# Kernel optimization log

Hardware: AMD Instinct MI355X
Metric: run time of the kernel (lower is better)

The kernel has to match this reference:

```python
import jax, jax.numpy as jnp
import numpy as np

N_NODES = 50000
N_EDGES = 300000
ANNOT = 200
HID = 256
N_STEPS = 8
N_BRANCH = 2


def setup_inputs() -> dict:
    key = jax.random.key(0)
    ks = jax.random.split(key, 12)
    s = 0.05
    return {
        "x": jax.random.normal(ks[0], (N_NODES, ANNOT), dtype=jnp.float32),
        "edge_index": jax.random.randint(ks[1], (2, N_EDGES), 0, N_NODES, dtype=jnp.int32),
        "batch": jnp.zeros((N_NODES,), dtype=jnp.int32),
        "W_reduce": jax.random.normal(ks[2], (HID, ANNOT), dtype=jnp.float32) * s,
        "b_reduce": jnp.zeros((HID,), dtype=jnp.float32),
        "W_ggc": jax.random.normal(ks[3], (N_STEPS, HID, HID), dtype=jnp.float32) * s,
        "W_ih": jax.random.normal(ks[4], (3 * HID, HID), dtype=jnp.float32) * s,
        "W_hh": jax.random.normal(ks[5], (3 * HID, HID), dtype=jnp.float32) * s,
        "b_ih": jnp.zeros((3 * HID,), dtype=jnp.float32),
        "b_hh": jnp.zeros((3 * HID,), dtype=jnp.float32),
        "W_lin": jax.random.normal(ks[6], (N_BRANCH, HID), dtype=jnp.float32) * s,
        "b_lin": jnp.zeros((N_BRANCH,), dtype=jnp.float32),
    }


def _gru_cell(m, h, W_ih, W_hh, b_ih, b_hh):
    # PyTorch GRUCell: gates ordered r, z, n
    gi = m @ W_ih.T + b_ih  # [N, 3H]
    gh = h @ W_hh.T + b_hh
    i_r, i_z, i_n = jnp.split(gi, 3, axis=1)
    h_r, h_z, h_n = jnp.split(gh, 3, axis=1)
    r = jax.nn.sigmoid(i_r + h_r)
    z = jax.nn.sigmoid(i_z + h_z)
    n = jnp.tanh(i_n + r * h_n)
    return (1.0 - z) * n + z * h


def reference(x, edge_index, batch, W_reduce, b_reduce, W_ggc, W_ih, W_hh, b_ih, b_hh, W_lin, b_lin):
    del batch  # unused by forward math
    n = x.shape[0]
    src, dst = edge_index[0], edge_index[1]

    h = x @ W_reduce.T + b_reduce  # [N, H]

    def step(h, Wi):
        m = h @ Wi                                    # per-step linear [N, H]
        agg = jax.ops.segment_sum(m[src], dst, num_segments=n)  # scatter-add to targets
        h_new = _gru_cell(agg, h, W_ih, W_hh, b_ih, b_hh)
        return h_new, None

    h, _ = jax.lax.scan(step, h, W_ggc)

    out = jax.nn.relu(h) @ W_lin.T + b_lin  # [N, 2]
    return jax.nn.log_softmax(out, axis=1)
```

## Files before the change

kernel.cpp:

```cpp
#include <hip/hip_runtime.h>

typedef _Float16 f16;
typedef unsigned short u16;
typedef unsigned int u32;
typedef _Float16 f16x4 __attribute__((ext_vector_type(4)));
typedef _Float16 f16x8 __attribute__((ext_vector_type(8)));
typedef float    floatx4 __attribute__((ext_vector_type(4)));

#define N_NODES 50000
#define N_EDGES 300000
#define ANNOT   200
#define KXP     224
#define HID     256

__device__ __forceinline__ floatx4 mfma_16x16x32_f16(f16x8 a, f16x8 b, floatx4 c) {
#if defined(__HIP_DEVICE_COMPILE__)
    return __builtin_amdgcn_mfma_f32_16x16x32_f16(a, b, c, 0, 0, 0);
#else
    return c;
#endif
}
__device__ __forceinline__ void gload_lds16(const f16* g, f16* l) {
#if defined(__HIP_DEVICE_COMPILE__)
    __builtin_amdgcn_global_load_lds((const __attribute__((address_space(1))) void*)g,
                                     (__attribute__((address_space(3))) void*)l, 16, 0, 0);
#else
    (void)g; (void)l;
#endif
}

__device__ __forceinline__ float sigm(float x) { return 1.0f / (1.0f + __expf(-x)); }
__device__ __forceinline__ float tanh_fast(float x) { return 1.0f - 2.0f / (1.0f + __expf(2.0f * x)); }

__device__ __forceinline__ float bf_bits_to_f32(u16 u) {
    union { u32 i; float f; } v; v.i = ((u32)u) << 16; return v.f;
}
__device__ __forceinline__ u16 f32_to_bf_bits(float f) {
    union { float f; u32 i; } v; v.f = f;
    u32 b = v.i;
    b += 0x7FFFu + ((b >> 16) & 1u);
    return (u16)(b >> 16);
}
__device__ __forceinline__ float load_in(const void* p, long i, int flag) {
    if (flag) return ((const float*)p)[i];
    return bf_bits_to_f32(((const u16*)p)[i]);
}

__global__ void probe_dtype(const u32* __restrict__ xw, int* __restrict__ flag) {
    __shared__ int cnt;
    if (threadIdx.x == 0) cnt = 0;
    __syncthreads();
    int c = 0;
    for (int i = threadIdx.x; i < 256; i += 64) {
        u32 lo = xw[i] & 0xFFFFu;
        u32 e = (lo >> 7) & 0xFFu;
        if (e >= 105u && e <= 140u) c++;
    }
    atomicAdd(&cnt, c);
    __syncthreads();
    if (threadIdx.x == 0) flag[0] = (cnt > 128) ? 0 : 1;
}

__global__ void cvt_f16(const void* __restrict__ in, f16* __restrict__ out, int n,
                        const int* __restrict__ flagp) {
    const int flag = *flagp;
    const int i = blockIdx.x * 256 + threadIdx.x;
    if (i < n) out[i] = (f16)load_in(in, i, flag);
}

__global__ void build_wrT(const void* __restrict__ Wre, f16* __restrict__ WrT,
                          const int* __restrict__ flagp) {
    const int flag = *flagp;
    const int i = blockIdx.x * 256 + threadIdx.x;
    if (i >= 256 * KXP) return;
    const int n = i / KXP, k = i - n * KXP;
    WrT[i] = (k < ANNOT) ? (f16)load_in(Wre, (long)n * ANNOT + k, flag) : (f16)0.0f;
}

__global__ void build_bb8(const f16* __restrict__ Wc, const void* __restrict__ Whh,
                          f16* __restrict__ Bb, const int* __restrict__ flagp) {
    const int flag = *flagp;
    const int i = blockIdx.x * 256 + threadIdx.x;
    const int s = i >> 19;
    const int rem = i & 524287;
    const int row = rem >> 9;
    const int k = rem & 511;
    const int chblk = row >> 7;
    const int r = row & 127;
    const int g = r >> 5;
    const int c = r & 31;
    const int ch = chblk * 32 + c;
    f16 v = (f16)0.0f;
    if (g == 0) {
        v = (k < 256) ? Wc[(long)ch * 2048 + s * 256 + k]
                      : (f16)load_in(Whh, (long)ch * 256 + (k - 256), flag);
    } else if (g == 1) {
        v = (k < 256) ? Wc[(long)(256 + ch) * 2048 + s * 256 + k]
                      : (f16)load_in(Whh, (long)(256 + ch) * 256 + (k - 256), flag);
    } else if (g == 2) {
        if (k < 256) v = Wc[(long)(512 + ch) * 2048 + s * 256 + k];
    } else {
        if (k >= 256) v = (f16)load_in(Whh, (long)(512 + ch) * 256 + (k - 256), flag);
    }
    Bb[i] = v;
}

__global__ void build_small(const void* b_ih, const void* b_hh, const void* b_red,
                            const void* W_lin, const void* b_lin,
                            float* __restrict__ sp, const int* __restrict__ flagp) {
    const int flag = *flagp;
    const int i = blockIdx.x * 256 + threadIdx.x;
    if (i < 512) {
        sp[i] = load_in(b_ih, i, flag) + load_in(b_hh, i, flag);
    } else if (i < 768) {
        sp[i] = load_in(b_ih, 512 + (i - 512), flag);
    } else if (i < 1024) {
        sp[i] = load_in(b_hh, 512 + (i - 768), flag);
    } else if (i < 1280) {
        sp[i] = load_in(b_red, i - 1024, flag);
    } else if (i < 1792) {
        sp[i] = load_in(W_lin, i - 1280, flag);
    } else if (i < 1794) {
        sp[i] = load_in(b_lin, i - 1792, flag);
    }
}

__global__ void build_xcvt(const void* __restrict__ x, f16* __restrict__ xc,
                           const int* __restrict__ flagp) {
    const int flag = *flagp;
    const long i = (long)blockIdx.x * 256 + threadIdx.x;
    if (i >= (long)N_NODES * KXP) return;
    const long r = i / KXP;
    const int  k = (int)(i - r * KXP);
    xc[i] = (k < ANNOT) ? (f16)load_in(x, r * ANNOT + k, flag) : (f16)0.0f;
}

__global__ void zero_i32(int* __restrict__ p, int n) {
    const int i = blockIdx.x * 256 + threadIdx.x;
    if (i < n) p[i] = 0;
}
__global__ void hist_kernel(const int* __restrict__ dst, int* __restrict__ deg, int n) {
    const int e = blockIdx.x * 256 + threadIdx.x;
    if (e < n) atomicAdd(&deg[dst[e]], 1);
}
__global__ void block_sum(const int* __restrict__ deg, int* __restrict__ partial, int n) {
    __shared__ int s[256];
    const int i = blockIdx.x * 256 + threadIdx.x;
    s[threadIdx.x] = (i < n) ? deg[i] : 0;
    __syncthreads();
    for (int off = 128; off > 0; off >>= 1) {
        if (threadIdx.x < off) s[threadIdx.x] += s[threadIdx.x + off];
        __syncthreads();
    }
    if (threadIdx.x == 0) partial[blockIdx.x] = s[0];
}
__global__ void scan_partials(int* __restrict__ partial, int nb, int* __restrict__ total_out) {
    __shared__ int s[256];
    const int t = threadIdx.x;
    s[t] = (t < nb) ? partial[t] : 0;
    __syncthreads();
    for (int off = 1; off < 256; off <<= 1) {
        int v = (t >= off) ? s[t - off] : 0;
        __syncthreads();
        s[t] += v;
        __syncthreads();
    }
    if (t < nb) partial[t] = (t == 0) ? 0 : s[t - 1];
    if (t == 0) *total_out = s[255];
}
__global__ void scan_block(const int* __restrict__ deg, const int* __restrict__ partial,
                           int* __restrict__ row_off, int* __restrict__ cursor, int n) {
    __shared__ int s[256];
    const int t = threadIdx.x;
    const int i = blockIdx.x * 256 + t;
    const int v = (i < n) ? deg[i] : 0;
    s[t] = v;
    __syncthreads();
    for (int off = 1; off < 256; off <<= 1) {
        int u = (t >= off) ? s[t - off] : 0;
        __syncthreads();
        s[t] += u;
        __syncthreads();
    }
    if (i < n) {
        const int v0 = partial[blockIdx.x] + s[t] - v;
        row_off[i] = v0;
        cursor[i]  = v0;
    }
}
__global__ void fill_kernel(const int* __restrict__ src, const int* __restrict__ dst,
                            int* __restrict__ cursor, int* __restrict__ csr, int n) {
    const int e = blockIdx.x * 256 + threadIdx.x;
    if (e < n) {
        const int p = atomicAdd(&cursor[dst[e]], 1);
        csr[p] = src[e];
    }
}

__global__ __launch_bounds__(256) void mgemm(
    const f16* __restrict__ A, int lda,
    const f16* __restrict__ Bt, int ldb,
    f16* __restrict__ C, int ldc,
    const float* __restrict__ bias,
    int M, int N, int K)
{
    __shared__ __attribute__((aligned(16))) f16 As[128 * 32];
    __shared__ __attribute__((aligned(16))) f16 Bs[128 * 32];
    const int tid  = threadIdx.x;
    const int lane = tid & 63;
    const int wave = tid >> 6;
    const int bm = blockIdx.x * 128;
    const int bn = blockIdx.y * 128;
    const int wm = (wave >> 1) * 64;
    const int wn = (wave & 1) * 64;
    const int quad = lane >> 4;
    const int l16  = lane & 15;

    floatx4 acc[4][4];
#pragma unroll
    for (int i = 0; i < 4; ++i)
#pragma unroll
        for (int j = 0; j < 4; ++j) acc[i][j] = (floatx4)(0.0f);

    for (int k0 = 0; k0 < K; k0 += 32) {
        __syncthreads();
#pragma unroll
        for (int it = 0; it < 2; ++it) {
            const int ci  = it * 256 + tid;
            const int row = ci >> 2;
            const int cg  = ci & 3;
            int ga = bm + row; if (ga > M - 1) ga = M - 1;
            gload_lds16(A + (long)ga * lda + k0 + cg * 8, As + ci * 8);
            gload_lds16(Bt + (long)(bn + row) * ldb + k0 + cg * 8, Bs + ci * 8);
        }
        __syncthreads();

        f16x8 af[4], bfv[4];
#pragma unroll
        for (int i = 0; i < 4; ++i) {
            af[i]  = *(const f16x8*)(As + (wm + i * 16 + l16) * 32 + quad * 8);
            bfv[i] = *(const f16x8*)(Bs + (wn + i * 16 + l16) * 32 + quad * 8);
        }
#pragma unroll
        for (int i = 0; i < 4; ++i)
#pragma unroll
            for (int j = 0; j < 4; ++j)
                acc[i][j] = mfma_16x16x32_f16(af[i], bfv[j], acc[i][j]);
    }

#pragma unroll
    for (int i = 0; i < 4; ++i) {
        const int r0 = bm + wm + i * 16 + quad * 4;
#pragma unroll
        for (int j = 0; j < 4; ++j) {
            const int col = bn + wn + j * 16 + l16;
            const float bv = bias ? bias[col] : 0.0f;
#pragma unroll
            for (int v = 0; v < 4; ++v) {
                const int r = r0 + v;
                if (r < M) C[(long)r * ldc + col] = (f16)(acc[i][j][v] + bv);
            }
        }
    }
}

__global__ __launch_bounds__(256) void gemm_gates(
    const f16* __restrict__ agh, const f16* __restrict__ Bb,
    f16* __restrict__ agh_nxt,
    const float* __restrict__ brz, const float* __restrict__ bin,
    const float* __restrict__ bhn, int M)
{
    __shared__ __attribute__((aligned(16))) f16 As[128 * 32];
    __shared__ __attribute__((aligned(16))) f16 Bs[128 * 32];
    const int tid  = threadIdx.x;
    const int lane = tid & 63;
    const int wave = tid >> 6;
    const int bm = blockIdx.y * 128;
    const int by = blockIdx.x;
    const int wm  = (wave >> 1) * 64;
    const int chh = (wave & 1) * 16;
    const int quad = lane >> 4;
    const int l16  = lane & 15;

    floatx4 acc[4][4];
#pragma unroll
    for (int i = 0; i < 4; ++i)
#pragma unroll
        for (int j = 0; j < 4; ++j) acc[i][j] = (floatx4)(0.0f);

    for (int k0 = 0; k0 < 512; k0 += 32) {
        __syncthreads();
#pragma unroll
        for (int it = 0; it < 2; ++it) {
            const int ci  = it * 256 + tid;
            const int row = ci >> 2;
            const int cg  = ci & 3;
            int ga = bm + row; if (ga > M - 1) ga = M - 1;
            gload_lds16(agh + (long)ga * 512 + k0 + cg * 8, As + ci * 8);
            gload_lds16(Bb + (long)(by * 128 + row) * 512 + k0 + cg * 8, Bs + ci * 8);
        }
        __syncthreads();

        f16x8 af[4], bfv[4];
#pragma unroll
        for (int i = 0; i < 4; ++i) {
            af[i]  = *(const f16x8*)(As + (wm + i * 16 + l16) * 32 + quad * 8);
            bfv[i] = *(const f16x8*)(Bs + (i * 32 + chh + l16) * 32 + quad * 8);
        }
#pragma unroll
        for (int i = 0; i < 4; ++i)
#pragma unroll
            for (int j = 0; j < 4; ++j)
                acc[i][j] = mfma_16x16x32_f16(af[i], bfv[j], acc[i][j]);
    }

    const int ch = by * 32 + chh + l16;
    const float b_r  = brz[ch];
    const float b_z  = brz[256 + ch];
    const float b_in = bin[ch];
    const float b_hn = bhn[ch];
#pragma unroll
    for (int i = 0; i < 4; ++i) {
        const int r0 = bm + wm + i * 16 + quad * 4;
#pragma unroll
        for (int v = 0; v < 4; ++v) {
            const int r = r0 + v;
            if (r < M) {
                const float rg = sigm(acc[i][0][v] + b_r);
                const float zg = sigm(acc[i][1][v] + b_z);
                const float nn = tanh_fast(acc[i][2][v] + b_in + rg * (acc[i][3][v] + b_hn));
                const float ho = (float)agh[(long)r * 512 + 256 + ch];
                agh_nxt[(long)r * 512 + 256 + ch] = (f16)((1.0f - zg) * nn + zg * ho);
            }
        }
    }
}

__global__ __launch_bounds__(256) void aggregate(
    f16* __restrict__ agh, const int* __restrict__ row_off, const int* __restrict__ csr)
{
    const int node = blockIdx.x * 4 + (threadIdx.x >> 6);
    const int lane = threadIdx.x & 63;
    if (node >= N_NODES) return;
    const int e0 = row_off[node], e1 = row_off[node + 1];
    float a0 = 0.0f, a1 = 0.0f, a2 = 0.0f, a3 = 0.0f;
    for (int e = e0; e < e1; ++e) {
        const int s = csr[e];
        const f16x4 v = *(const f16x4*)(agh + (long)s * 512 + 256 + lane * 4);
        a0 += (float)v[0]; a1 += (float)v[1]; a2 += (float)v[2]; a3 += (float)v[3];
    }
    f16x4 o;
    o[0] = (f16)a0; o[1] = (f16)a1; o[2] = (f16)a2; o[3] = (f16)a3;
    *(f16x4*)(agh + (long)node * 512 + lane * 4) = o;
}

__global__ __launch_bounds__(256) void final_kernel(
    const f16* __restrict__ h, const float* __restrict__ wlin,
    const float* __restrict__ blin, void* __restrict__ out,
    const int* __restrict__ flagp)
{
    const int flag = *flagp;
    const int node = blockIdx.x * 4 + (threadIdx.x >> 6);
    const int lane = threadIdx.x & 63;
    if (node >= N_NODES) return;
    const f16* hp = h + (long)node * 512;
    float a0 = 0.0f, a1 = 0.0f;
#pragma unroll
    for (int u = 0; u < 4; ++u) {
        const int c = lane * 4 + u;
        float hv = (float)hp[c];
        hv = hv > 0.0f ? hv : 0.0f;
        a0 += hv * wlin[c];
        a1 += hv * wlin[256 + c];
    }
#pragma unroll
    for (int off = 32; off > 0; off >>= 1) {
        a0 += __shfl_down(a0, off);
        a1 += __shfl_down(a1, off);
    }
    if (lane == 0) {
        a0 += blin[0];
        a1 += blin[1];
        const float mx  = fmaxf(a0, a1);
        const float lse = mx + logf(expf(a0 - mx) + expf(a1 - mx));
        const float o0 = a0 - lse, o1 = a1 - lse;
        if (flag) {
            ((float*)out)[(long)node * 2]     = o0;
            ((float*)out)[(long)node * 2 + 1] = o1;
        } else {
            ((u16*)out)[(long)node * 2]     = f32_to_bf_bits(o0);
            ((u16*)out)[(long)node * 2 + 1] = f32_to_bf_bits(o1);
        }
    }
}

extern "C" void kernel_launch(void* const* d_in, const int* in_sizes, int n_in,
                              void* d_out, int out_size, void* d_ws, size_t ws_size,
                              hipStream_t stream)
{
    (void)in_sizes; (void)n_in; (void)out_size; (void)ws_size;
    const void* x        = d_in[0];
    const int*  ei       = (const int*)d_in[1];
    const void* W_reduce = d_in[3];
    const void* b_reduce = d_in[4];
    const void* W_ggc    = d_in[5];
    const void* W_ih     = d_in[6];
    const void* W_hh     = d_in[7];
    const void* b_ih     = d_in[8];
    const void* b_hh     = d_in[9];
    const void* W_lin    = d_in[10];
    const void* b_lin    = d_in[11];
    const int* src = ei;
    const int* dst = ei + N_EDGES;

    char* w = (char*)d_ws;
    auto carve = [&](size_t bytes) -> char* {
        char* p = w;
        w += (bytes + 255) & ~(size_t)255;
        return p;
    };
    f16* agh_a = (f16*)carve((size_t)N_NODES * 512 * 2);
    f16* agh_b = (f16*)carve((size_t)N_NODES * 512 * 2);
    f16* x_cvt = agh_b;
    f16*   WrT   = (f16*)carve((size_t)256 * KXP * 2);
    f16*   Wih16 = (f16*)carve((size_t)768 * 256 * 2);
    f16*   Wg16  = (f16*)carve((size_t)2048 * 256 * 2);
    f16*   Wc    = (f16*)carve((size_t)768 * 2048 * 2);
    f16*   Bb8   = (f16*)carve((size_t)8 * 1024 * 512 * 2);
    float* sp    = (float*)carve(2048 * 4);
    int*   flag  = (int*)carve(256);
    int* deg     = (int*)carve((size_t)N_NODES * 4);
    int* row_off = (int*)carve((size_t)(N_NODES + 1) * 4);
    int* cursor  = (int*)carve((size_t)N_NODES * 4);
    int* csr     = (int*)carve((size_t)N_EDGES * 4);
    int* partial = (int*)carve(256 * 4);

    float* brz  = sp;
    float* bin  = sp + 512;
    float* bhn  = sp + 768;
    float* br0  = sp + 1024;
    float* wlin = sp + 1280;
    float* blin = sp + 1792;

    probe_dtype<<<1, 64, 0, stream>>>((const u32*)x, flag);

    cvt_f16<<<(768 * 256 + 255) / 256, 256, 0, stream>>>(W_ih, Wih16, 768 * 256, flag);
    cvt_f16<<<(2048 * 256 + 255) / 256, 256, 0, stream>>>(W_ggc, Wg16, 2048 * 256, flag);
    build_wrT<<<(256 * KXP + 255) / 256, 256, 0, stream>>>(W_reduce, WrT, flag);
    build_small<<<8, 256, 0, stream>>>(b_ih, b_hh, b_reduce, W_lin, b_lin, sp, flag);
    build_xcvt<<<(int)(((long)N_NODES * KXP + 255) / 256), 256, 0, stream>>>(x, x_cvt, flag);

    zero_i32<<<196, 256, 0, stream>>>(deg, N_NODES);
    hist_kernel<<<(N_EDGES + 255) / 256, 256, 0, stream>>>(dst, deg, N_EDGES);
    block_sum<<<196, 256, 0, stream>>>(deg, partial, N_NODES);
    scan_partials<<<1, 256, 0, stream>>>(partial, 196, row_off + N_NODES);
    scan_block<<<196, 256, 0, stream>>>(deg, partial, row_off, cursor, N_NODES);
    fill_kernel<<<(N_EDGES + 255) / 256, 256, 0, stream>>>(src, dst, cursor, csr, N_EDGES);

    mgemm<<<dim3(6, 16), 256, 0, stream>>>(Wih16, 256, Wg16, 256, Wc, 2048,
                                           (const float*)nullptr, 768, 2048, 256);
    build_bb8<<<(8 * 1024 * 512) / 256, 256, 0, stream>>>(Wc, W_hh, Bb8, flag);

    mgemm<<<dim3(391, 2), 256, 0, stream>>>(x_cvt, KXP, WrT, KXP, agh_a + 256, 512, br0,
                                            N_NODES, 256, KXP);

    for (int s = 0; s < 8; ++s) {
        f16* cur = (s & 1) ? agh_b : agh_a;
        f16* nxt = (s & 1) ? agh_a : agh_b;
        aggregate<<<12500, 256, 0, stream>>>(cur, row_off, csr);
        gemm_gates<<<dim3(8, 391), 256, 0, stream>>>(cur, Bb8 + (size_t)s * 524288, nxt,
                                                     brz, bin, bhn, N_NODES);
    }

    final_kernel<<<12500, 256, 0, stream>>>(agh_a + 256, wlin, blin, d_out, flag);
}
```

Baseline: 1.306 ms.

## Swizzle gate-GEMM blocks, reuse LDS h tile, widen aggregate loads

The gate GEMM now uses a 1D grid remapped so that groups of 8 row blocks share all 8 column blocks. This is meant to improve L2 reuse of the A rows. The old h value for the GRU update is now captured from the already-staged LDS A tile instead of being re-read from global memory. The aggregate kernel uses 32 lanes per node with 16-byte loads instead of 64 lanes with 8-byte loads. This halves the block count and widens each gather, at the cost of more accumulator registers.

```diff
diff --git a/kernel.cpp b/kernel.cpp
--- a/kernel.cpp
+++ b/kernel.cpp
@@ -270,23 +270,30 @@
     const float* __restrict__ brz, const float* __restrict__ bin,
     const float* __restrict__ bhn, int M)
 {
+    const int lin = blockIdx.x;
+    const int within = lin & 63;
+    const int rb = (lin >> 6) * 8 + (within & 7);
+    const int cb = within >> 3;
+    if (rb * 128 >= M) return;
+
     __shared__ __attribute__((aligned(16))) f16 As[128 * 32];
     __shared__ __attribute__((aligned(16))) f16 Bs[128 * 32];
     const int tid  = threadIdx.x;
     const int lane = tid & 63;
     const int wave = tid >> 6;
-    const int bm = blockIdx.y * 128;
-    const int by = blockIdx.x;
+    const int bm = rb * 128;
     const int wm  = (wave >> 1) * 64;
     const int chh = (wave & 1) * 16;
     const int quad = lane >> 4;
     const int l16  = lane & 15;
+    const int k_cap = 256 + cb * 32;
 
     floatx4 acc[4][4];
 #pragma unroll
     for (int i = 0; i < 4; ++i)
 #pragma unroll
         for (int j = 0; j < 4; ++j) acc[i][j] = (floatx4)(0.0f);
+    f16 h_frag[4][4] = {};
 
     for (int k0 = 0; k0 < 512; k0 += 32) {
         __syncthreads();
@@ -297,9 +304,17 @@
             const int cg  = ci & 3;
             int ga = bm + row; if (ga > M - 1) ga = M - 1;
             gload_lds16(agh + (long)ga * 512 + k0 + cg * 8, As + ci * 8);
-            gload_lds16(Bb + (long)(by * 128 + row) * 512 + k0 + cg * 8, Bs + ci * 8);
-        }
-        __syncthreads();
+            gload_lds16(Bb + (long)(cb * 128 + row) * 512 + k0 + cg * 8, Bs + ci * 8);
+        }
+        __syncthreads();
+
+        if (k0 == k_cap) {
+#pragma unroll
+            for (int i = 0; i < 4; ++i)
+#pragma unroll
+                for (int v = 0; v < 4; ++v)
+                    h_frag[i][v] = As[(wm + i * 16 + quad * 4 + v) * 32 + chh + l16];
+        }
 
         f16x8 af[4], bfv[4];
 #pragma unroll
@@ -314,7 +329,7 @@
                 acc[i][j] = mfma_16x16x32_f16(af[i], bfv[j], acc[i][j]);
     }
 
-    const int ch = by * 32 + chh + l16;
+    const int ch = cb * 32 + chh + l16;
     const float b_r  = brz[ch];
     const float b_z  = brz[256 + ch];
     const float b_in = bin[ch];
@@ -329,7 +344,7 @@
                 const float rg = sigm(acc[i][0][v] + b_r);
                 const float zg = sigm(acc[i][1][v] + b_z);
                 const float nn = tanh_fast(acc[i][2][v] + b_in + rg * (acc[i][3][v] + b_hn));
-                const float ho = (float)agh[(long)r * 512 + 256 + ch];
+                const float ho = (float)h_frag[i][v];
                 agh_nxt[(long)r * 512 + 256 + ch] = (f16)((1.0f - zg) * nn + zg * ho);
             }
         }
@@ -339,19 +354,21 @@
 __global__ __launch_bounds__(256) void aggregate(
     f16* __restrict__ agh, const int* __restrict__ row_off, const int* __restrict__ csr)
 {
-    const int node = blockIdx.x * 4 + (threadIdx.x >> 6);
-    const int lane = threadIdx.x & 63;
+    const int node = blockIdx.x * 8 + (threadIdx.x >> 5);
+    const int lane = threadIdx.x & 31;
     if (node >= N_NODES) return;
     const int e0 = row_off[node], e1 = row_off[node + 1];
-    float a0 = 0.0f, a1 = 0.0f, a2 = 0.0f, a3 = 0.0f;
+    float a[8] = {0.0f, 0.0f, 0.0f, 0.0f, 0.0f, 0.0f, 0.0f, 0.0f};
     for (int e = e0; e < e1; ++e) {
         const int s = csr[e];
-        const f16x4 v = *(const f16x4*)(agh + (long)s * 512 + 256 + lane * 4);
-        a0 += (float)v[0]; a1 += (float)v[1]; a2 += (float)v[2]; a3 += (float)v[3];
-    }
-    f16x4 o;
-    o[0] = (f16)a0; o[1] = (f16)a1; o[2] = (f16)a2; o[3] = (f16)a3;
-    *(f16x4*)(agh + (long)node * 512 + lane * 4) = o;
+        const f16x8 v = *(const f16x8*)(agh + (long)s * 512 + 256 + lane * 8);
+#pragma unroll
+        for (int u = 0; u < 8; ++u) a[u] += (float)v[u];
+    }
+    f16x8 o;
+#pragma unroll
+    for (int u = 0; u < 8; ++u) o[u] = (f16)a[u];
+    *(f16x8*)(agh + (long)node * 512 + lane * 8) = o;
 }
 
 __global__ __launch_bounds__(256) void final_kernel(
@@ -467,9 +484,9 @@
     for (int s = 0; s < 8; ++s) {
         f16* cur = (s & 1) ? agh_b : agh_a;
         f16* nxt = (s & 1) ? agh_a : agh_b;
-        aggregate<<<12500, 256, 0, stream>>>(cur, row_off, csr);
-        gemm_gates<<<dim3(8, 391), 256, 0, stream>>>(cur, Bb8 + (size_t)s * 524288, nxt,
-                                                     brz, bin, bhn, N_NODES);
+        aggregate<<<6250, 256, 0, stream>>>(cur, row_off, csr);
+        gemm_gates<<<49 * 64, 256, 0, stream>>>(cur, Bb8 + (size_t)s * 524288, nxt,
+                                                brz, bin, bhn, N_NODES);
     }
 
     final_kernel<<<12500, 256, 0, stream>>>(agh_a + 256, wlin, blin, d_out, flag);
```

Measured after the change: 1.265 ms. 1.03x faster.
